# Performance work log

Hardware: AMD Instinct MI355X
Metric: run time of the kernel (lower is better)

The kernel has to match this reference:

```python
import jax, jax.numpy as jnp
import numpy as np
from jax.scipy.special import logsumexp

D, V, B, N = 256, 10000, 16, 22
CF, CR, CA = 400, 120, 48   # num_func_cats, num_res_cats, num_arg_cats
NEG = -1e9


def setup_inputs() -> dict:
    key = jax.random.key(0)
    ks = jax.random.split(key, 12)
    s = 0.1
    return {
        "fake_emb": jnp.eye(CR, dtype=jnp.float32),  # nn.Parameter(torch.eye(num_res_cats))
        "nt_emb": jax.random.normal(ks[0], (CF, D), jnp.float32),
        "rule_W": jax.random.normal(ks[1], (2 * CA, CR), jnp.float32) * s,
        "rule_b": jnp.zeros((2 * CA,), jnp.float32),
        "root_w": jax.random.normal(ks[2], (CF,), jnp.float32) * s,  # root_mlp weight (input dim 1)
        "root_b": jnp.zeros((CF,), jnp.float32),
        "root_mask": jnp.zeros((CF,), jnp.float32),  # can_be_root mask (0 = allowed)
        "split_W1": jax.random.normal(ks[3], (D, D), jnp.float32) * s,
        "split_b1": jnp.zeros((D,), jnp.float32),
        "res_W": jax.random.normal(ks[4], (2, 2, D, D), jnp.float32) * s,  # 2 ResidualLayers x 2 Linears
        "res_b": jnp.zeros((2, 2, D), jnp.float32),
        "split_Wo": jax.random.normal(ks[5], (D, 2), jnp.float32) * s,
        "split_bo": jnp.zeros((2,), jnp.float32),
        "emit_W": jax.random.normal(ks[6], (D, V), jnp.float32) * s,  # word emission head
        "emit_b": jnp.zeros((V,), jnp.float32),
        "words": jax.random.randint(ks[7], (B, N), 0, V),
        "lfunc_ixs": jax.random.randint(ks[8], (CR, CA), 0, CF),
        "rfunc_ixs": jax.random.randint(ks[9], (CR, CA), 0, CF),
    }


def reference(fake_emb, nt_emb, rule_W, rule_b, root_w, root_b, root_mask,
              split_W1, split_b1, res_W, res_b, split_Wo, split_bo,
              emit_W, emit_b, words, lfunc_ixs, rfunc_ixs):
    # ---- grammar scores (set_grammar branch) ----
    # root_mlp(eye(1)).squeeze() == root_w + root_b
    root_scores = jax.nn.log_softmax(root_mask + root_w + root_b)          # [CF]
    rule_scores = jax.nn.log_softmax(fake_emb @ rule_W.T + rule_b, axis=1)  # [CR, 2*CA]

    # split_mlp: Linear -> ResidualLayer x2 -> Linear(D,2)
    h = nt_emb @ split_W1 + split_b1
    for i in range(2):  # fixed small layer loop
        t = jax.nn.relu(h @ res_W[i, 0] + res_b[i, 0])
        h = jax.nn.relu(t @ res_W[i, 1] + res_b[i, 1]) + h
    split_scores = jax.nn.log_softmax(h @ split_Wo + split_bo, axis=1)      # [CF, 2]

    gL = rule_scores[:, :CA] + split_scores[:CR, 0:1]  # full_G_larg [CR, CA]
    gR = rule_scores[:, CA:] + split_scores[:CR, 0:1]  # full_G_rarg [CR, CA]

    # ---- emission model: log p(word | category) gathered per token ----
    word_lp = jax.nn.log_softmax(nt_emb @ emit_W + emit_b, axis=-1)  # [CF, V]
    emit = word_lp[:, words]                                         # [CF, B, N]
    term = (split_scores[:, 1][:, None, None] + emit).transpose(2, 1, 0)  # [N, B, CF]

    # ---- CKY inside pass: beta[i, j, b, cat] over spans ----
    beta = jnp.full((N, N, B, CF), NEG, jnp.float32)
    d = jnp.arange(N)
    beta = beta.at[d, d].set(term)

    for w in range(2, N + 1):  # recurrence over span widths (static)
        S = N - w + 1
        st = np.arange(S)[:, None]          # span starts [S,1]
        kk = np.arange(1, w)[None, :]       # split points [1,w-1]
        left = beta[st, st + kk - 1]                                   # [S,w-1,B,CF]
        right = beta[st + kk, np.broadcast_to(st + w - 1, (S, w - 1))]  # [S,w-1,B,CF]
        # res -> arg(left) + rfunc(right)
        sL = gL + left[..., :CA][..., None, :] + right[..., rfunc_ixs]  # [S,w-1,B,CR,CA]
        # res -> lfunc(left) + arg(right)
        sR = gR + left[..., lfunc_ixs] + right[..., :CA][..., None, :]
        new = jnp.logaddexp(logsumexp(sL, axis=(1, 4)),
                            logsumexp(sR, axis=(1, 4)))                 # [S,B,CR]
        full = jnp.full((S, B, CF), NEG, jnp.float32).at[..., :CR].set(new)
        beta = beta.at[st[:, 0], st[:, 0] + w - 1].set(full)

    ll = logsumexp(root_scores + beta[0, N - 1], axis=-1)  # [B]
    return -ll  # logprob_list * -1
```

## Files before the change

### kernel.cpp

```cpp
#include <hip/hip_runtime.h>
#include <math.h>

#define D 256
#define V 10000
#define BB 16
#define NN 22
#define CF 400
#define CR 120
#define CA 48
#define CRP 121
#define PADF 20

__global__ __launch_bounds__(512) void k_mlp(const float* __restrict__ nt_emb, const float* __restrict__ W1,
                      const float* __restrict__ b1, const float* __restrict__ resW,
                      const float* __restrict__ resb, const float* __restrict__ Wo,
                      const float* __restrict__ bo, float* __restrict__ split_scores) {
  __shared__ float xs[2][D], hs[2][D], ts[2][D], prt[2][2][D];
  __shared__ float redg[2][4][2];
  int t = threadIdx.x; int c = t & 255; int h = t >> 8;
  int f0 = blockIdx.x * 2;
  xs[h][c] = nt_emb[(size_t)(f0 + h) * D + c];
  __syncthreads();
  int d0 = h * 128;
  float a0 = 0.f, a1 = 0.f;
#pragma unroll 8
  for (int dd = 0; dd < 128; dd++) {
    float wv = W1[(size_t)(d0 + dd) * D + c];
    a0 += xs[0][d0 + dd] * wv; a1 += xs[1][d0 + dd] * wv;
  }
  prt[0][h][c] = a0; prt[1][h][c] = a1;
  __syncthreads();
  if (h == 0) {
    float bv = b1[c];
    hs[0][c] = prt[0][0][c] + prt[0][1][c] + bv;
    hs[1][c] = prt[1][0][c] + prt[1][1][c] + bv;
  }
  __syncthreads();
  for (int il = 0; il < 2; il++) {
    const float* W = resW + (size_t)(il * 2) * D * D;
    a0 = 0.f; a1 = 0.f;
#pragma unroll 8
    for (int dd = 0; dd < 128; dd++) {
      float wv = W[(size_t)(d0 + dd) * D + c];
      a0 += hs[0][d0 + dd] * wv; a1 += hs[1][d0 + dd] * wv;
    }
    prt[0][h][c] = a0; prt[1][h][c] = a1;
    __syncthreads();
    if (h == 0) {
      float bv = resb[(il * 2) * D + c];
      ts[0][c] = fmaxf(prt[0][0][c] + prt[0][1][c] + bv, 0.f);
      ts[1][c] = fmaxf(prt[1][0][c] + prt[1][1][c] + bv, 0.f);
    }
    __syncthreads();
    const float* W2 = resW + (size_t)(il * 2 + 1) * D * D;
    a0 = 0.f; a1 = 0.f;
#pragma unroll 8
    for (int dd = 0; dd < 128; dd++) {
      float wv = W2[(size_t)(d0 + dd) * D + c];
      a0 += ts[0][d0 + dd] * wv; a1 += ts[1][d0 + dd] * wv;
    }
    prt[0][h][c] = a0; prt[1][h][c] = a1;
    __syncthreads();
    if (h == 0) {
      float bv = resb[(il * 2 + 1) * D + c];
      hs[0][c] = fmaxf(prt[0][0][c] + prt[0][1][c] + bv, 0.f) + hs[0][c];
      hs[1][c] = fmaxf(prt[1][0][c] + prt[1][1][c] + bv, 0.f) + hs[1][c];
    }
    __syncthreads();
  }
  float y0 = hs[h][c] * Wo[c * 2 + 0], y1 = hs[h][c] * Wo[c * 2 + 1];
  for (int off = 32; off; off >>= 1) { y0 += __shfl_down(y0, off, 64); y1 += __shfl_down(y1, off, 64); }
  int wq = (t >> 6) & 3;
  if ((t & 63) == 0) { redg[h][wq][0] = y0; redg[h][wq][1] = y1; }
  __syncthreads();
  if (c == 0) {
    float s0 = redg[h][0][0] + redg[h][1][0] + redg[h][2][0] + redg[h][3][0] + bo[0];
    float s1 = redg[h][0][1] + redg[h][1][1] + redg[h][2][1] + redg[h][3][1] + bo[1];
    float m = fmaxf(s0, s1);
    float z = m + __logf(__expf(s0 - m) + __expf(s1 - m));
    split_scores[(f0 + h) * 2 + 0] = s0 - z;
    split_scores[(f0 + h) * 2 + 1] = s1 - z;
  }
}

#define RT 16
__global__ __launch_bounds__(128) void k_emit_partial(const float* __restrict__ nt_emb,
                               const float* __restrict__ emit_W,
                               const float* __restrict__ emit_b, float* __restrict__ partial) {
  __shared__ float xs[RT][D];
  __shared__ float ldsw[RT][2];
  int bid = blockIdx.x;
  int xcd = bid & 7;
  int n = bid >> 3;
  int xt = n % 25;
  int yh = n / 25;
  int y = yh * 8 + xcd;
  if (y >= 20) return;
  int t = threadIdx.x;
  int f0 = xt * RT;
  int v0 = y * 512 + t * 4;
  for (int idx = t; idx < RT * D; idx += 128) {
    int ri = idx >> 8, d = idx & 255;
    xs[ri][d] = nt_emb[(size_t)(f0 + ri) * D + d];
  }
  __syncthreads();
  float acc[RT][4];
#pragma unroll
  for (int ri = 0; ri < RT; ri++)
    for (int j = 0; j < 4; j++) acc[ri][j] = 0.f;
#pragma unroll 2
  for (int d4 = 0; d4 < D / 4; d4++) {
    float4 w0 = *(const float4*)(emit_W + (size_t)(4 * d4 + 0) * V + v0);
    float4 w1 = *(const float4*)(emit_W + (size_t)(4 * d4 + 1) * V + v0);
    float4 w2 = *(const float4*)(emit_W + (size_t)(4 * d4 + 2) * V + v0);
    float4 w3 = *(const float4*)(emit_W + (size_t)(4 * d4 + 3) * V + v0);
#pragma unroll
    for (int ri = 0; ri < RT; ri++) {
      float4 xv = *(const float4*)(&xs[ri][4 * d4]);
      acc[ri][0] += xv.x * w0.x + xv.y * w1.x + xv.z * w2.x + xv.w * w3.x;
      acc[ri][1] += xv.x * w0.y + xv.y * w1.y + xv.z * w2.y + xv.w * w3.y;
      acc[ri][2] += xv.x * w0.z + xv.y * w1.z + xv.z * w2.z + xv.w * w3.z;
      acc[ri][3] += xv.x * w0.w + xv.y * w1.w + xv.z * w2.w + xv.w * w3.w;
    }
  }
  float4 eb = *(const float4*)(emit_b + v0);
  float psum[RT];
#pragma unroll
  for (int ri = 0; ri < RT; ri++)
    psum[ri] = __expf(acc[ri][0] + eb.x) + __expf(acc[ri][1] + eb.y) +
               __expf(acc[ri][2] + eb.z) + __expf(acc[ri][3] + eb.w);
  int lane = t & 63, wid = t >> 6;
  for (int ri = 0; ri < RT; ri++) {
    float v = psum[ri];
    for (int off = 32; off; off >>= 1) v += __shfl_down(v, off, 64);
    if (lane == 0) ldsw[ri][wid] = v;
  }
  __syncthreads();
  if (t < RT) partial[(f0 + t) * 32 + y] = ldsw[t][0] + ldsw[t][1];
}

__global__ void k_glgr(const float* __restrict__ rule_W, const float* __restrict__ rule_b,
                       const float* __restrict__ split_scores,
                       const int* __restrict__ lf, const int* __restrict__ rf,
                       const float* __restrict__ partialE, float* __restrict__ logZ,
                       float4* __restrict__ rules) {
  __shared__ float red[128];
  __shared__ float shv[96];
  int r = blockIdx.x;
  int t = threadIdx.x;
  if (r == CR) {
    for (int f = t; f < CF; f += 128) {
      float s = 0.f;
      for (int ct = 0; ct < 20; ct++) s += partialE[f * 32 + ct];
      logZ[f] = __logf(s);
    }
    return;
  }
  float x = (t < 96) ? (rule_W[t * CR + r] + rule_b[t]) : -INFINITY;
  red[t] = x; __syncthreads();
  for (int off = 64; off; off >>= 1) { if (t < off) red[t] = fmaxf(red[t], red[t + off]); __syncthreads(); }
  float m = red[0]; __syncthreads();
  red[t] = (t < 96) ? __expf(x - m) : 0.f; __syncthreads();
  for (int off = 64; off; off >>= 1) { if (t < off) red[t] += red[t + off]; __syncthreads(); }
  float z = m + __logf(red[0]);
  float s0 = split_scores[r * 2 + 0];
  if (t < 96) shv[t] = __expf((x - z) + s0);
  __syncthreads();
  if (t < CA) {
    float4 pk;
    pk.x = shv[t];
    pk.y = shv[CA + t];
    pk.z = __int_as_float(rf[r * CA + t]);
    pk.w = __int_as_float(lf[r * CA + t]);
    rules[r * CA + t] = pk;
  }
}

__global__ __launch_bounds__(512) void k_term(const float* __restrict__ nt_emb,
                       const float* __restrict__ emit_W,
                       const float* __restrict__ emit_b, const int* __restrict__ words,
                       const float* __restrict__ split_scores, const float* __restrict__ logZ,
                       float* __restrict__ ET, float* __restrict__ bmax) {
  __shared__ float vals[CF];
  __shared__ float redw[8];
  __shared__ float mfin;
  int blk = blockIdx.x;
  int b = blk / NN, n = blk % NN;
  int t = threadIdx.x;
  int lane = t & 63, wid = t >> 6;
  int wd = words[b * NN + n];
  float wc0 = emit_W[(size_t)(4 * lane + 0) * V + wd];
  float wc1 = emit_W[(size_t)(4 * lane + 1) * V + wd];
  float wc2 = emit_W[(size_t)(4 * lane + 2) * V + wd];
  float wc3 = emit_W[(size_t)(4 * lane + 3) * V + wd];
  float eb = emit_b[wd];
  float vmax = -INFINITY;
  int fbase = wid * 50;
  for (int k = 0; k < 50; k += 2) {
    int f0 = fbase + k, f1 = f0 + 1;
    float4 xa = *(const float4*)(nt_emb + (size_t)f0 * D + 4 * lane);
    float4 xb = *(const float4*)(nt_emb + (size_t)f1 * D + 4 * lane);
    float va = xa.x * wc0 + xa.y * wc1 + xa.z * wc2 + xa.w * wc3;
    float vb = xb.x * wc0 + xb.y * wc1 + xb.z * wc2 + xb.w * wc3;
    for (int off = 32; off; off >>= 1) {
      va += __shfl_down(va, off, 64);
      vb += __shfl_down(vb, off, 64);
    }
    if (lane == 0) {
      float fa = split_scores[f0 * 2 + 1] + (va + eb) - logZ[f0];
      float fb = split_scores[f1 * 2 + 1] + (vb + eb) - logZ[f1];
      vals[f0] = fa; vals[f1] = fb;
      vmax = fmaxf(vmax, fmaxf(fa, fb));
    }
  }
  if (lane == 0) redw[wid] = vmax;
  __syncthreads();
  if (t == 0) {
    float m = redw[0];
    for (int i2 = 1; i2 < 8; i2++) m = fmaxf(m, redw[i2]);
    mfin = m;
    bmax[(n * NN + n) * BB + b] = m;
  }
  __syncthreads();
  float m = mfin;
  for (int f = t; f < CF; f += 512) ET[((size_t)n * CF + f) * BB + b] = __expf(vals[f] - m);
}

__global__ __launch_bounds__(512) void k_cky_part(const float4* __restrict__ rules,
                      const float* __restrict__ ET, const float* __restrict__ EB,
                      const float* __restrict__ bmax, float* __restrict__ partial,
                      int w, int rsplit) {
  __shared__ float SL[CF * PADF];
  __shared__ float SR[CF * PADF];
  __shared__ float sMbuf[21 * BB];
  __shared__ float cks[BB];
  __shared__ float4 sred[512];
  int t = threadIdx.x;
  int blk = blockIdx.x;
  int rb = blk % rsplit; int rem = blk / rsplit;
  int wm1 = w - 1;
  int k = rem % wm1; int s = rem / wm1;
  int i = s, j = s + w - 1;
  bool ld = (k == 0), rd = (k == wm1 - 1);
  if (t < BB * wm1) {
    int k2 = t >> 4, b2 = t & 15;
    sMbuf[t] = bmax[(i * NN + (i + k2)) * BB + b2] + bmax[((i + k2 + 1) * NN + j) * BB + b2];
  }
  __syncthreads();
  if (t < BB) {
    float M = sMbuf[t];
    for (int k2 = 1; k2 < wm1; k2++) M = fmaxf(M, sMbuf[k2 * BB + t]);
    cks[t] = __expf(sMbuf[k * BB + t] - M);
  }
  const float* srcL = ld ? (ET + (size_t)i * CF * BB) : (EB + (size_t)(i * NN + (i + k)) * CRP * BB);
  const float* srcR = rd ? (ET + (size_t)j * CF * BB) : (EB + (size_t)((i + k + 1) * NN + j) * CRP * BB);
  int rowsL = ld ? CF : CRP, rowsR = rd ? CF : CRP;
  for (int idx = t; idx < rowsL * 4; idx += 512) {
    int f = idx >> 2, q = idx & 3;
    *(float4*)&SL[f * PADF + q * 4] = *(const float4*)&srcL[f * BB + q * 4];
  }
  for (int idx = t; idx < rowsR * 4; idx += 512) {
    int f = idx >> 2, q = idx & 3;
    *(float4*)&SR[f * PADF + q * 4] = *(const float4*)&srcR[f * BB + q * 4];
  }
  __syncthreads();
  int nr = CR / rsplit;
  int asplit = 128 / nr;
  int bq = t & 3, rr = t >> 2;
  float4 acc = {0.f, 0.f, 0.f, 0.f};
  bool act = (rr < nr * asplit);
  int rloc = rr % nr, asub = rr / nr;
  int r = rb * nr + rloc;
  if (act) {
    int na = CA / asplit;
    const float4* rp = rules + (size_t)r * CA + asub * na;
    int boff = bq * 4;
    int aB = asub * na;
#pragma unroll 4
    for (int a0 = 0; a0 < na; a0++) {
      float4 rule = rp[a0];
      int a = aB + a0;
      int fL = __float_as_int(rule.z);
      int fR = __float_as_int(rule.w);
      int fLc = rd ? fL : min(fL, 120);
      int fRc = ld ? fR : min(fR, 120);
      float4 La = *(const float4*)&SL[a * PADF + boff];
      float4 Ra = *(const float4*)&SR[a * PADF + boff];
      float4 Rg = *(const float4*)&SR[fLc * PADF + boff];
      float4 Lg = *(const float4*)&SL[fRc * PADF + boff];
      acc.x += rule.x * (La.x * Rg.x) + rule.y * (Lg.x * Ra.x);
      acc.y += rule.x * (La.y * Rg.y) + rule.y * (Lg.y * Ra.y);
      acc.z += rule.x * (La.z * Rg.z) + rule.y * (Lg.z * Ra.z);
      acc.w += rule.x * (La.w * Rg.w) + rule.y * (Lg.w * Ra.w);
    }
  }
  if (asplit > 1) {
    sred[t] = acc;
    __syncthreads();
    if (act && asub == 0) {
      for (int s2 = 1; s2 < asplit; s2++) {
        float4 o = sred[t + s2 * nr * 4];
        acc.x += o.x; acc.y += o.y; acc.z += o.z; acc.w += o.w;
      }
    }
  }
  if (act && asub == 0) {
    float4 c4 = *(const float4*)&cks[bq * 4];
    acc.x *= c4.x; acc.y *= c4.y; acc.z *= c4.z; acc.w *= c4.w;
    *(float4*)&partial[(((size_t)s * 21 + k) * CR + r) * BB + bq * 4] = acc;
  }
}

__global__ __launch_bounds__(512) void k_cky_comb(const float* __restrict__ partial,
                      float* __restrict__ EB, float* __restrict__ bmax, int w) {
  __shared__ float sums[CR * BB];
  __shared__ float sMbuf[21 * BB];
  __shared__ float msum[BB];
  __shared__ float Mb[BB];
  int t = threadIdx.x;
  int s = blockIdx.x;
  int i = s, j = s + w - 1;
  int wm1 = w - 1;
  if (t < BB * wm1) {
    int k2 = t >> 4, b2 = t & 15;
    sMbuf[t] = bmax[(i * NN + (i + k2)) * BB + b2] + bmax[((i + k2 + 1) * NN + j) * BB + b2];
  }
  __syncthreads();
  if (t < BB) {
    float M = sMbuf[t];
    for (int k2 = 1; k2 < wm1; k2++) M = fmaxf(M, sMbuf[k2 * BB + t]);
    Mb[t] = M;
  }
  int bq = t & 3, rr = t >> 2;
  float4 sum = {0.f, 0.f, 0.f, 0.f};
  if (rr < CR) {
    for (int k2 = 0; k2 < wm1; k2++) {
      float4 p = *(const float4*)&partial[(((size_t)s * 21 + k2) * CR + rr) * BB + bq * 4];
      sum.x += p.x; sum.y += p.y; sum.z += p.z; sum.w += p.w;
    }
    *(float4*)&sums[rr * BB + bq * 4] = sum;
  }
  __syncthreads();
  if (t < BB) {
    float m = 0.f;
    for (int r2 = 0; r2 < CR; r2++) m = fmaxf(m, sums[r2 * BB + t]);
    m = fmaxf(m, 1e-35f);
    msum[t] = m;
    bmax[(i * NN + j) * BB + t] = Mb[t] + __logf(m);
  }
  __syncthreads();
  if (rr < CR) {
    float4 m4 = *(const float4*)&msum[bq * 4];
    sum.x /= m4.x; sum.y /= m4.y; sum.z /= m4.z; sum.w /= m4.w;
    *(float4*)&EB[(((size_t)i * NN + j) * CRP + rr) * BB + bq * 4] = sum;
  }
  if (t < BB) EB[(((size_t)i * NN + j) * CRP + 120) * BB + t] = 0.f;
}

__global__ __launch_bounds__(128) void k_final(const float* __restrict__ root_w,
                        const float* __restrict__ root_b, const float* __restrict__ root_mask,
                        const float* __restrict__ EB, const float* __restrict__ bmax,
                        float* __restrict__ out) {
  __shared__ float red[128];
  int b = blockIdx.x;
  int t = threadIdx.x;
  float xv[4];
  float lm = -INFINITY;
  for (int kq = 0; kq < 4; kq++) {
    int f = t + kq * 128;
    xv[kq] = (f < CF) ? (root_mask[f] + root_w[f] + root_b[f]) : -INFINITY;
    lm = fmaxf(lm, xv[kq]);
  }
  red[t] = lm; __syncthreads();
  for (int off = 64; off; off >>= 1) { if (t < off) red[t] = fmaxf(red[t], red[t + off]); __syncthreads(); }
  float M = red[0]; __syncthreads();
  float le = 0.f;
  for (int kq = 0; kq < 4; kq++) le += (t + kq * 128 < CF) ? __expf(xv[kq] - M) : 0.f;
  red[t] = le; __syncthreads();
  for (int off = 64; off; off >>= 1) { if (t < off) red[t] += red[t + off]; __syncthreads(); }
  float z = M + __logf(red[0]);
  __syncthreads();
  float x = (t < CR) ? __expf(xv[0] - z) * EB[(((size_t)0 * NN + (NN - 1)) * CRP + t) * BB + b] : 0.f;
  red[t] = x; __syncthreads();
  for (int off = 64; off; off >>= 1) { if (t < off) red[t] += red[t + off]; __syncthreads(); }
  if (t == 0) out[b] = -(bmax[(0 * NN + (NN - 1)) * BB + b] + __logf(red[0]));
}

extern "C" void kernel_launch(void* const* d_in, const int* in_sizes, int n_in,
                              void* d_out, int out_size, void* d_ws, size_t ws_size,
                              hipStream_t stream) {
  const float* nt_emb   = (const float*)d_in[1];
  const float* rule_W   = (const float*)d_in[2];
  const float* rule_b   = (const float*)d_in[3];
  const float* root_w   = (const float*)d_in[4];
  const float* root_b   = (const float*)d_in[5];
  const float* root_mask= (const float*)d_in[6];
  const float* split_W1 = (const float*)d_in[7];
  const float* split_b1 = (const float*)d_in[8];
  const float* res_W    = (const float*)d_in[9];
  const float* res_b    = (const float*)d_in[10];
  const float* split_Wo = (const float*)d_in[11];
  const float* split_bo = (const float*)d_in[12];
  const float* emit_W   = (const float*)d_in[13];
  const float* emit_b   = (const float*)d_in[14];
  const int*   words    = (const int*)d_in[15];
  const int*   lfunc    = (const int*)d_in[16];
  const int*   rfunc    = (const int*)d_in[17];

  float* ws = (float*)d_ws;
  float* ET           = ws;
  float* EB           = ET + NN * CF * BB;
  float* bmaxbuf      = EB + NN * NN * CRP * BB;
  float* partialK     = bmaxbuf + NN * NN * BB;
  float* rules        = partialK + 21 * 21 * CR * BB;
  float* split_scores = rules + CR * CA * 4;
  float* logZ         = split_scores + 2 * CF;
  float* partialE     = logZ + CF;

  hipLaunchKernelGGL(k_mlp, dim3(CF / 2), dim3(512), 0, stream, nt_emb, split_W1, split_b1,
                     res_W, res_b, split_Wo, split_bo, split_scores);
  hipLaunchKernelGGL(k_emit_partial, dim3(600), dim3(128), 0, stream, nt_emb, emit_W, emit_b, partialE);
  hipLaunchKernelGGL(k_glgr, dim3(CR + 1), dim3(128), 0, stream, rule_W, rule_b, split_scores,
                     lfunc, rfunc, partialE, logZ, (float4*)rules);
  hipLaunchKernelGGL(k_term, dim3(BB * NN), dim3(512), 0, stream, nt_emb, emit_W, emit_b,
                     words, split_scores, logZ, ET, bmaxbuf);
  for (int w = 2; w <= NN; w++) {
    int S = NN - w + 1;
    int units = S * (w - 1);
    int rsplit = (units >= 224) ? 1 : ((units >= 112) ? 2 : ((units >= 56) ? 4 : 8));
    hipLaunchKernelGGL(k_cky_part, dim3(units * rsplit), dim3(512), 0, stream,
                       (const float4*)rules, ET, EB, bmaxbuf, partialK, w, rsplit);
    hipLaunchKernelGGL(k_cky_comb, dim3(S), dim3(512), 0, stream, partialK, EB, bmaxbuf, w);
  }
  hipLaunchKernelGGL(k_final, dim3(BB), dim3(128), 0, stream, root_w, root_b, root_mask,
                     EB, bmaxbuf, (float*)d_out);
}
```

Measured before the change: 394.1 us.

## Fuse CKY width loop into one cooperative persistent kernel with grid syncs

Replaces the per-width pair of CKY kernel launches (42 launches) with a single cooperative kernel of 256 persistent blocks that loops over span widths and uses grid.sync between the partial and combine phases. This removes per-launch overhead and the tail of many small grids. It also halves the row tile of the emission-partition kernel and doubles its grid. The risk is that grid-wide barriers cost more than kernel boundaries, and that rsplit selection now depends on the fixed grid size.

```diff
diff --git a/kernel.cpp b/kernel.cpp
--- a/kernel.cpp
+++ b/kernel.cpp
@@ -1,5 +1,8 @@
 #include <hip/hip_runtime.h>
+#include <hip/hip_cooperative_groups.h>
 #include <math.h>
+
+namespace cg = cooperative_groups;
 
 #define D 256
 #define V 10000
@@ -10,6 +13,7 @@
 #define CA 48
 #define CRP 121
 #define PADF 20
+#define GCOOP 256
 
 __global__ __launch_bounds__(512) void k_mlp(const float* __restrict__ nt_emb, const float* __restrict__ W1,
                       const float* __restrict__ b1, const float* __restrict__ resW,
@@ -83,7 +87,7 @@
   }
 }
 
-#define RT 16
+#define RT 8
 __global__ __launch_bounds__(128) void k_emit_partial(const float* __restrict__ nt_emb,
                                const float* __restrict__ emit_W,
                                const float* __restrict__ emit_b, float* __restrict__ partial) {
@@ -92,8 +96,8 @@
   int bid = blockIdx.x;
   int xcd = bid & 7;
   int n = bid >> 3;
-  int xt = n % 25;
-  int yh = n / 25;
+  int xt = n % 50;
+  int yh = n / 50;
   int y = yh * 8 + xcd;
   if (y >= 20) return;
   int t = threadIdx.x;
@@ -104,31 +108,34 @@
     xs[ri][d] = nt_emb[(size_t)(f0 + ri) * D + d];
   }
   __syncthreads();
-  float acc[RT][4];
+  float psum[RT];
+  for (int ri = 0; ri < RT; ri++) psum[ri] = 0.f;
+  if (v0 < V) {
+    float acc[RT][4];
 #pragma unroll
-  for (int ri = 0; ri < RT; ri++)
-    for (int j = 0; j < 4; j++) acc[ri][j] = 0.f;
+    for (int ri = 0; ri < RT; ri++)
+      for (int j = 0; j < 4; j++) acc[ri][j] = 0.f;
 #pragma unroll 2
-  for (int d4 = 0; d4 < D / 4; d4++) {
-    float4 w0 = *(const float4*)(emit_W + (size_t)(4 * d4 + 0) * V + v0);
-    float4 w1 = *(const float4*)(emit_W + (size_t)(4 * d4 + 1) * V + v0);
-    float4 w2 = *(const float4*)(emit_W + (size_t)(4 * d4 + 2) * V + v0);
-    float4 w3 = *(const float4*)(emit_W + (size_t)(4 * d4 + 3) * V + v0);
+    for (int d4 = 0; d4 < D / 4; d4++) {
+      float4 w0 = *(const float4*)(emit_W + (size_t)(4 * d4 + 0) * V + v0);
+      float4 w1 = *(const float4*)(emit_W + (size_t)(4 * d4 + 1) * V + v0);
+      float4 w2 = *(const float4*)(emit_W + (size_t)(4 * d4 + 2) * V + v0);
+      float4 w3 = *(const float4*)(emit_W + (size_t)(4 * d4 + 3) * V + v0);
 #pragma unroll
-    for (int ri = 0; ri < RT; ri++) {
-      float4 xv = *(const float4*)(&xs[ri][4 * d4]);
-      acc[ri][0] += xv.x * w0.x + xv.y * w1.x + xv.z * w2.x + xv.w * w3.x;
-      acc[ri][1] += xv.x * w0.y + xv.y * w1.y + xv.z * w2.y + xv.w * w3.y;
-      acc[ri][2] += xv.x * w0.z + xv.y * w1.z + xv.z * w2.z + xv.w * w3.z;
-      acc[ri][3] += xv.x * w0.w + xv.y * w1.w + xv.z * w2.w + xv.w * w3.w;
-    }
-  }
-  float4 eb = *(const float4*)(emit_b + v0);
-  float psum[RT];
+      for (int ri = 0; ri < RT; ri++) {
+        float4 xv = *(const float4*)(&xs[ri][4 * d4]);
+        acc[ri][0] += xv.x * w0.x + xv.y * w1.x + xv.z * w2.x + xv.w * w3.x;
+        acc[ri][1] += xv.x * w0.y + xv.y * w1.y + xv.z * w2.y + xv.w * w3.y;
+        acc[ri][2] += xv.x * w0.z + xv.y * w1.z + xv.z * w2.z + xv.w * w3.z;
+        acc[ri][3] += xv.x * w0.w + xv.y * w1.w + xv.z * w2.w + xv.w * w3.w;
+      }
+    }
+    float4 eb = *(const float4*)(emit_b + v0);
 #pragma unroll
-  for (int ri = 0; ri < RT; ri++)
-    psum[ri] = __expf(acc[ri][0] + eb.x) + __expf(acc[ri][1] + eb.y) +
-               __expf(acc[ri][2] + eb.z) + __expf(acc[ri][3] + eb.w);
+    for (int ri = 0; ri < RT; ri++)
+      psum[ri] = __expf(acc[ri][0] + eb.x) + __expf(acc[ri][1] + eb.y) +
+                 __expf(acc[ri][2] + eb.z) + __expf(acc[ri][3] + eb.w);
+  }
   int lane = t & 63, wid = t >> 6;
   for (int ri = 0; ri < RT; ri++) {
     float v = psum[ri];
@@ -226,135 +233,139 @@
   for (int f = t; f < CF; f += 512) ET[((size_t)n * CF + f) * BB + b] = __expf(vals[f] - m);
 }
 
-__global__ __launch_bounds__(512) void k_cky_part(const float4* __restrict__ rules,
-                      const float* __restrict__ ET, const float* __restrict__ EB,
-                      const float* __restrict__ bmax, float* __restrict__ partial,
-                      int w, int rsplit) {
+__global__ __launch_bounds__(512) void k_cky_coop(const float4* __restrict__ rules,
+                      const float* __restrict__ ET, float* __restrict__ EB,
+                      float* __restrict__ bmax, float* __restrict__ partial) {
+  cg::grid_group grid = cg::this_grid();
   __shared__ float SL[CF * PADF];
   __shared__ float SR[CF * PADF];
   __shared__ float sMbuf[21 * BB];
   __shared__ float cks[BB];
   __shared__ float4 sred[512];
+  __shared__ float Mb[BB];
+  __shared__ float msum[BB];
+  float* sums = SL;
   int t = threadIdx.x;
-  int blk = blockIdx.x;
-  int rb = blk % rsplit; int rem = blk / rsplit;
-  int wm1 = w - 1;
-  int k = rem % wm1; int s = rem / wm1;
-  int i = s, j = s + w - 1;
-  bool ld = (k == 0), rd = (k == wm1 - 1);
-  if (t < BB * wm1) {
-    int k2 = t >> 4, b2 = t & 15;
-    sMbuf[t] = bmax[(i * NN + (i + k2)) * BB + b2] + bmax[((i + k2 + 1) * NN + j) * BB + b2];
-  }
-  __syncthreads();
-  if (t < BB) {
-    float M = sMbuf[t];
-    for (int k2 = 1; k2 < wm1; k2++) M = fmaxf(M, sMbuf[k2 * BB + t]);
-    cks[t] = __expf(sMbuf[k * BB + t] - M);
-  }
-  const float* srcL = ld ? (ET + (size_t)i * CF * BB) : (EB + (size_t)(i * NN + (i + k)) * CRP * BB);
-  const float* srcR = rd ? (ET + (size_t)j * CF * BB) : (EB + (size_t)((i + k + 1) * NN + j) * CRP * BB);
-  int rowsL = ld ? CF : CRP, rowsR = rd ? CF : CRP;
-  for (int idx = t; idx < rowsL * 4; idx += 512) {
-    int f = idx >> 2, q = idx & 3;
-    *(float4*)&SL[f * PADF + q * 4] = *(const float4*)&srcL[f * BB + q * 4];
-  }
-  for (int idx = t; idx < rowsR * 4; idx += 512) {
-    int f = idx >> 2, q = idx & 3;
-    *(float4*)&SR[f * PADF + q * 4] = *(const float4*)&srcR[f * BB + q * 4];
-  }
-  __syncthreads();
-  int nr = CR / rsplit;
-  int asplit = 128 / nr;
   int bq = t & 3, rr = t >> 2;
-  float4 acc = {0.f, 0.f, 0.f, 0.f};
-  bool act = (rr < nr * asplit);
-  int rloc = rr % nr, asub = rr / nr;
-  int r = rb * nr + rloc;
-  if (act) {
-    int na = CA / asplit;
-    const float4* rp = rules + (size_t)r * CA + asub * na;
-    int boff = bq * 4;
-    int aB = asub * na;
+
+  for (int w = 2; w <= NN; w++) {
+    int wm1 = w - 1;
+    int S = NN - w + 1;
+    int units = S * wm1;
+    int rsplit = (units * 8 <= GCOOP) ? 8 : ((units * 4 <= GCOOP) ? 4 : ((units * 2 <= GCOOP) ? 2 : 1));
+    int tot = units * rsplit;
+    for (int blk = blockIdx.x; blk < tot; blk += GCOOP) {
+      int rb = blk % rsplit; int rem = blk / rsplit;
+      int k = rem % wm1; int s = rem / wm1;
+      int i = s, j = s + w - 1;
+      bool ld = (k == 0), rd = (k == wm1 - 1);
+      if (t < BB * wm1) {
+        int k2 = t >> 4, b2 = t & 15;
+        sMbuf[t] = bmax[(i * NN + (i + k2)) * BB + b2] + bmax[((i + k2 + 1) * NN + j) * BB + b2];
+      }
+      __syncthreads();
+      if (t < BB) {
+        float M = sMbuf[t];
+        for (int k2 = 1; k2 < wm1; k2++) M = fmaxf(M, sMbuf[k2 * BB + t]);
+        cks[t] = __expf(sMbuf[k * BB + t] - M);
+      }
+      const float* srcL = ld ? (ET + (size_t)i * CF * BB) : (EB + (size_t)(i * NN + (i + k)) * CRP * BB);
+      const float* srcR = rd ? (ET + (size_t)j * CF * BB) : (EB + (size_t)((i + k + 1) * NN + j) * CRP * BB);
+      int rowsL = ld ? CF : CRP, rowsR = rd ? CF : CRP;
+      for (int idx = t; idx < rowsL * 4; idx += 512) {
+        int f = idx >> 2, q = idx & 3;
+        *(float4*)&SL[f * PADF + q * 4] = *(const float4*)&srcL[f * BB + q * 4];
+      }
+      for (int idx = t; idx < rowsR * 4; idx += 512) {
+        int f = idx >> 2, q = idx & 3;
+        *(float4*)&SR[f * PADF + q * 4] = *(const float4*)&srcR[f * BB + q * 4];
+      }
+      __syncthreads();
+      int nr = CR / rsplit;
+      int asplit = 128 / nr;
+      float4 acc = {0.f, 0.f, 0.f, 0.f};
+      bool act = (rr < nr * asplit);
+      int rloc = rr % nr, asub = rr / nr;
+      int r = rb * nr + rloc;
+      if (act) {
+        int na = CA / asplit;
+        const float4* rp = rules + (size_t)r * CA + asub * na;
+        int boff = bq * 4;
 #pragma unroll 4
-    for (int a0 = 0; a0 < na; a0++) {
-      float4 rule = rp[a0];
-      int a = aB + a0;
-      int fL = __float_as_int(rule.z);
-      int fR = __float_as_int(rule.w);
-      int fLc = rd ? fL : min(fL, 120);
-      int fRc = ld ? fR : min(fR, 120);
-      float4 La = *(const float4*)&SL[a * PADF + boff];
-      float4 Ra = *(const float4*)&SR[a * PADF + boff];
-      float4 Rg = *(const float4*)&SR[fLc * PADF + boff];
-      float4 Lg = *(const float4*)&SL[fRc * PADF + boff];
-      acc.x += rule.x * (La.x * Rg.x) + rule.y * (Lg.x * Ra.x);
-      acc.y += rule.x * (La.y * Rg.y) + rule.y * (Lg.y * Ra.y);
-      acc.z += rule.x * (La.z * Rg.z) + rule.y * (Lg.z * Ra.z);
-      acc.w += rule.x * (La.w * Rg.w) + rule.y * (Lg.w * Ra.w);
-    }
-  }
-  if (asplit > 1) {
-    sred[t] = acc;
-    __syncthreads();
-    if (act && asub == 0) {
-      for (int s2 = 1; s2 < asplit; s2++) {
-        float4 o = sred[t + s2 * nr * 4];
-        acc.x += o.x; acc.y += o.y; acc.z += o.z; acc.w += o.w;
-      }
-    }
-  }
-  if (act && asub == 0) {
-    float4 c4 = *(const float4*)&cks[bq * 4];
-    acc.x *= c4.x; acc.y *= c4.y; acc.z *= c4.z; acc.w *= c4.w;
-    *(float4*)&partial[(((size_t)s * 21 + k) * CR + r) * BB + bq * 4] = acc;
-  }
-}
-
-__global__ __launch_bounds__(512) void k_cky_comb(const float* __restrict__ partial,
-                      float* __restrict__ EB, float* __restrict__ bmax, int w) {
-  __shared__ float sums[CR * BB];
-  __shared__ float sMbuf[21 * BB];
-  __shared__ float msum[BB];
-  __shared__ float Mb[BB];
-  int t = threadIdx.x;
-  int s = blockIdx.x;
-  int i = s, j = s + w - 1;
-  int wm1 = w - 1;
-  if (t < BB * wm1) {
-    int k2 = t >> 4, b2 = t & 15;
-    sMbuf[t] = bmax[(i * NN + (i + k2)) * BB + b2] + bmax[((i + k2 + 1) * NN + j) * BB + b2];
-  }
-  __syncthreads();
-  if (t < BB) {
-    float M = sMbuf[t];
-    for (int k2 = 1; k2 < wm1; k2++) M = fmaxf(M, sMbuf[k2 * BB + t]);
-    Mb[t] = M;
-  }
-  int bq = t & 3, rr = t >> 2;
-  float4 sum = {0.f, 0.f, 0.f, 0.f};
-  if (rr < CR) {
-    for (int k2 = 0; k2 < wm1; k2++) {
-      float4 p = *(const float4*)&partial[(((size_t)s * 21 + k2) * CR + rr) * BB + bq * 4];
-      sum.x += p.x; sum.y += p.y; sum.z += p.z; sum.w += p.w;
-    }
-    *(float4*)&sums[rr * BB + bq * 4] = sum;
-  }
-  __syncthreads();
-  if (t < BB) {
-    float m = 0.f;
-    for (int r2 = 0; r2 < CR; r2++) m = fmaxf(m, sums[r2 * BB + t]);
-    m = fmaxf(m, 1e-35f);
-    msum[t] = m;
-    bmax[(i * NN + j) * BB + t] = Mb[t] + __logf(m);
-  }
-  __syncthreads();
-  if (rr < CR) {
-    float4 m4 = *(const float4*)&msum[bq * 4];
-    sum.x /= m4.x; sum.y /= m4.y; sum.z /= m4.z; sum.w /= m4.w;
-    *(float4*)&EB[(((size_t)i * NN + j) * CRP + rr) * BB + bq * 4] = sum;
-  }
-  if (t < BB) EB[(((size_t)i * NN + j) * CRP + 120) * BB + t] = 0.f;
+        for (int a0 = 0; a0 < na; a0++) {
+          float4 rule = rp[a0];
+          int a = asub * na + a0;
+          int fL = __float_as_int(rule.z);
+          int fR = __float_as_int(rule.w);
+          int fLc = rd ? fL : min(fL, 120);
+          int fRc = ld ? fR : min(fR, 120);
+          float4 La = *(const float4*)&SL[a * PADF + boff];
+          float4 Ra = *(const float4*)&SR[a * PADF + boff];
+          float4 Rg = *(const float4*)&SR[fLc * PADF + boff];
+          float4 Lg = *(const float4*)&SL[fRc * PADF + boff];
+          acc.x += rule.x * (La.x * Rg.x) + rule.y * (Lg.x * Ra.x);
+          acc.y += rule.x * (La.y * Rg.y) + rule.y * (Lg.y * Ra.y);
+          acc.z += rule.x * (La.z * Rg.z) + rule.y * (Lg.z * Ra.z);
+          acc.w += rule.x * (La.w * Rg.w) + rule.y * (Lg.w * Ra.w);
+        }
+      }
+      if (asplit > 1) {
+        sred[t] = acc;
+        __syncthreads();
+        if (act && asub == 0) {
+          for (int s2 = 1; s2 < asplit; s2++) {
+            float4 o = sred[t + s2 * nr * 4];
+            acc.x += o.x; acc.y += o.y; acc.z += o.z; acc.w += o.w;
+          }
+        }
+      }
+      if (act && asub == 0) {
+        float4 c4 = *(const float4*)&cks[bq * 4];
+        acc.x *= c4.x; acc.y *= c4.y; acc.z *= c4.z; acc.w *= c4.w;
+        *(float4*)&partial[(((size_t)s * 21 + k) * CR + r) * BB + bq * 4] = acc;
+      }
+      __syncthreads();
+    }
+    grid.sync();
+    for (int s = blockIdx.x; s < S; s += GCOOP) {
+      int i = s, j = s + w - 1;
+      if (t < BB * wm1) {
+        int k2 = t >> 4, b2 = t & 15;
+        sMbuf[t] = bmax[(i * NN + (i + k2)) * BB + b2] + bmax[((i + k2 + 1) * NN + j) * BB + b2];
+      }
+      __syncthreads();
+      if (t < BB) {
+        float M = sMbuf[t];
+        for (int k2 = 1; k2 < wm1; k2++) M = fmaxf(M, sMbuf[k2 * BB + t]);
+        Mb[t] = M;
+      }
+      float4 sum = {0.f, 0.f, 0.f, 0.f};
+      if (rr < CR) {
+        for (int k2 = 0; k2 < wm1; k2++) {
+          float4 p = *(const float4*)&partial[(((size_t)s * 21 + k2) * CR + rr) * BB + bq * 4];
+          sum.x += p.x; sum.y += p.y; sum.z += p.z; sum.w += p.w;
+        }
+        *(float4*)&sums[rr * BB + bq * 4] = sum;
+      }
+      __syncthreads();
+      if (t < BB) {
+        float m = 0.f;
+        for (int r2 = 0; r2 < CR; r2++) m = fmaxf(m, sums[r2 * BB + t]);
+        m = fmaxf(m, 1e-35f);
+        msum[t] = m;
+        bmax[(i * NN + j) * BB + t] = Mb[t] + __logf(m);
+      }
+      __syncthreads();
+      if (rr < CR) {
+        float4 m4 = *(const float4*)&msum[bq * 4];
+        sum.x /= m4.x; sum.y /= m4.y; sum.z /= m4.z; sum.w /= m4.w;
+        *(float4*)&EB[(((size_t)i * NN + j) * CRP + rr) * BB + bq * 4] = sum;
+      }
+      if (t < BB) EB[(((size_t)i * NN + j) * CRP + 120) * BB + t] = 0.f;
+      __syncthreads();
+    }
+    grid.sync();
+  }
 }
 
 __global__ __launch_bounds__(128) void k_final(const float* __restrict__ root_w,
@@ -419,18 +430,19 @@
 
   hipLaunchKernelGGL(k_mlp, dim3(CF / 2), dim3(512), 0, stream, nt_emb, split_W1, split_b1,
                      res_W, res_b, split_Wo, split_bo, split_scores);
-  hipLaunchKernelGGL(k_emit_partial, dim3(600), dim3(128), 0, stream, nt_emb, emit_W, emit_b, partialE);
+  hipLaunchKernelGGL(k_emit_partial, dim3(1200), dim3(128), 0, stream, nt_emb, emit_W, emit_b, partialE);
   hipLaunchKernelGGL(k_glgr, dim3(CR + 1), dim3(128), 0, stream, rule_W, rule_b, split_scores,
                      lfunc, rfunc, partialE, logZ, (float4*)rules);
   hipLaunchKernelGGL(k_term, dim3(BB * NN), dim3(512), 0, stream, nt_emb, emit_W, emit_b,
                      words, split_scores, logZ, ET, bmaxbuf);
-  for (int w = 2; w <= NN; w++) {
-    int S = NN - w + 1;
-    int units = S * (w - 1);
-    int rsplit = (units >= 224) ? 1 : ((units >= 112) ? 2 : ((units >= 56) ? 4 : 8));
-    hipLaunchKernelGGL(k_cky_part, dim3(units * rsplit), dim3(512), 0, stream,
-                       (const float4*)rules, ET, EB, bmaxbuf, partialK, w, rsplit);
-    hipLaunchKernelGGL(k_cky_comb, dim3(S), dim3(512), 0, stream, partialK, EB, bmaxbuf, w);
+  {
+    const float4* rules4 = (const float4*)rules;
+    const float* ETp = ET;
+    float* EBp = EB;
+    float* bmaxp = bmaxbuf;
+    float* partp = partialK;
+    void* kargs[5] = { (void*)&rules4, (void*)&ETp, (void*)&EBp, (void*)&bmaxp, (void*)&partp };
+    hipLaunchCooperativeKernel((const void*)k_cky_coop, dim3(GCOOP), dim3(512), kargs, 0, stream);
   }
   hipLaunchKernelGGL(k_final, dim3(BB), dim3(128), 0, stream, root_w, root_b, root_mask,
                      EB, bmaxbuf, (float*)d_out);
```

New measurement: 1.562 ms. +296.4%, slower.
